# Kernel optimization log

Measured on AMD Instinct MI355X. Metric: run time of the kernel, lower is better.

Reference implementation:

```python
import jax, jax.numpy as jnp
import numpy as np

B, H, L, TAU, THETA = 8192, 256, 4, 8, 8


def setup_inputs() -> dict:
    key = jax.random.key(0)
    ks = jax.random.split(key, 16)
    w = lambda k, shape: (jax.random.normal(k, shape, jnp.float32) * 0.02)
    return {
        "x": jax.random.normal(ks[0], (B, H), jnp.float32),
        "t_att": jax.random.normal(ks[1], (L, TAU, B, H), jnp.float32),
        "s_att": jax.random.normal(ks[2], (L, TAU, B, H), jnp.float32),
        "embed_w": w(ks[3], (H, H)),
        "embed_b": jnp.zeros((H,), jnp.float32),
        "wtn": w(ks[4], (L, H, H)),
        "btn": jnp.zeros((L, H), jnp.float32),
        "wsn": w(ks[5], (L, H, H)),
        "bsn": jnp.zeros((L, H), jnp.float32),
        "wt": w(ks[6], (L, 3 * H, H)),
        "bt": jnp.zeros((L, 3 * H), jnp.float32),
        "ws": w(ks[7], (L, 3 * H, H)),
        "bs": jnp.zeros((L, 3 * H), jnp.float32),
        "out_w": w(ks[8], (H, H)),
        "out_b": jnp.zeros((H,), jnp.float32),
    }


def _forward(x, t_att, s_att, embed_w, embed_b, wtn, btn, wsn, bsn, wt, bt, ws, bs, out_w, out_b):
    n_layers, tau = t_att.shape[0], t_att.shape[1]
    b, h = x.shape
    scale = 1.0 / np.sqrt(h).astype(np.float32)
    theta = THETA

    S = x @ embed_w.T + embed_b  # embed: [B, H]
    # rolling spatial buffers, start as theta zero entries
    t_sp = jnp.zeros((theta, b, h), x.dtype)
    s_sp = jnp.zeros((theta, b, h), x.dtype)

    for i in range(n_layers):
        T_last = t_att[i, -1]  # [B, H]
        # append current S_t / last T_t to spatial buffers, keep last theta
        s_sp = jnp.concatenate([s_sp[1:], S[None]], axis=0)
        t_sp = jnp.concatenate([t_sp[1:], T_last[None]], axis=0)
        # s_att[i].append(S_t); slice last tau -> keys include current S
        s_keys = jnp.concatenate([s_att[i, 1:], S[None]], axis=0)  # [tau, B, H]
        t_vals = t_att[i]  # [tau, B, H]

        s_next = S @ wsn[i].T + bsn[i]
        t_next = T_last @ wtn[i].T + btn[i]

        # temporal attention over last-tau history
        w_t = jax.nn.softmax(jnp.einsum('kbh,bh->kb', s_keys, s_next) * scale, axis=0)
        T_trend = jnp.einsum('kb,kbh->bh', w_t, t_vals)
        t_gate = jax.nn.sigmoid(t_next)
        T_fusion = T_last * t_gate + (1.0 - t_gate) * T_trend

        # spatial attention over last-theta buffer
        w_s = jax.nn.softmax(jnp.einsum('kbh,bh->kb', t_sp, t_next) * scale, axis=0)
        S_trend = jnp.einsum('kb,kbh->bh', w_s, s_sp)
        s_gate = jax.nn.sigmoid(s_next)
        S_fusion = S * s_gate + (1.0 - s_gate) * S_trend

        Tc = T_fusion @ wt[i].T + bt[i]  # [B, 3H]
        Sc = S_fusion @ ws[i].T + bs[i]
        t_g, t_t_, t_s_ = jnp.split(Tc, 3, axis=-1)
        s_g, s_t_, s_s_ = jnp.split(Sc, 3, axis=-1)
        Tg = jax.nn.sigmoid(t_g)
        Sg = jax.nn.sigmoid(s_g)
        # T_new feeds the (stateful) history; S carries to next layer
        S = Sg * s_s_ + (1.0 - Sg) * t_s_

    return jnp.tanh(S @ out_w.T + out_b)


def reference(x, t_att, s_att, embed_w, embed_b, wtn, btn, wsn, bsn, wt, bt, ws, bs, out_w, out_b):
    return _forward(x, t_att, s_att, embed_w, embed_b, wtn, btn, wsn, bsn, wt, bt, ws, bs, out_w, out_b)
```

## Files before the change

kernel.cpp:

```cpp
#include <hip/hip_runtime.h>
#include <cmath>

typedef __attribute__((ext_vector_type(8))) short short8;
typedef __attribute__((ext_vector_type(4))) float f32x4;
typedef __attribute__((ext_vector_type(4))) unsigned short us4;
typedef unsigned short u16;

#define BATCH 8192
#define HDIM  256
static constexpr size_t BH = (size_t)BATCH * HDIM;

__device__ __forceinline__ u16 f2bf(float f) {
    union { float f; unsigned u; } v; v.f = f;
    unsigned r = v.u + 0x7FFFu + ((v.u >> 16) & 1u);
    return (u16)(r >> 16);
}
__device__ __forceinline__ float bf2f(u16 u) {
    union { unsigned u; float f; } v; v.u = ((unsigned)u) << 16;
    return v.f;
}
__device__ __forceinline__ float wred(float v) {
#pragma unroll
    for (int o = 32; o > 0; o >>= 1) v += __shfl_xor(v, o);
    return v;
}
__device__ __forceinline__ float sigmoidf_(float x) {
    return 1.f / (1.f + __expf(-x));
}

__global__ __launch_bounds__(256) void convert_weights(
    const float* __restrict__ embed_w, const float* __restrict__ wtn,
    const float* __restrict__ wsn, const float* __restrict__ wt,
    const float* __restrict__ ws, const float* __restrict__ out_w,
    u16* __restrict__ dst)
{
    int idx = blockIdx.x * 256 + threadIdx.x;
    int e = idx * 4;
    if (e >= 22 * 65536) return;
    int c = e >> 16, o = e & 65535;
    const float* src;
    if (c == 0)      src = embed_w + o;
    else if (c < 5)  src = wtn + (size_t)(c - 1) * 65536 + o;
    else if (c < 9)  src = wsn + (size_t)(c - 5) * 65536 + o;
    else if (c < 13) src = wt + (size_t)(c - 9) * 768 * 256 + 512 * 256 + o;
    else if (c < 17) src = ws + (size_t)(c - 13) * 768 * 256 + o;
    else if (c < 21) src = ws + (size_t)(c - 17) * 768 * 256 + 512 * 256 + o;
    else             src = out_w + o;
    f32x4 v = *(const f32x4*)src;
    us4 r;
#pragma unroll
    for (int j = 0; j < 4; ++j) r[j] = f2bf(v[j]);
    *(us4*)(dst + e) = r;
}

template<bool A_F32, int ACT>
__global__ __launch_bounds__(256) void gemm256(
    const void* __restrict__ Ap, const u16* __restrict__ W,
    const float* __restrict__ bias, void* __restrict__ Cp)
{
    int lane = threadIdx.x & 63;
    int wave = threadIdx.x >> 6;
    int wm = wave >> 1, wn = wave & 1;
    int row0 = blockIdx.x * 128 + wm * 64;
    int col0 = blockIdx.y * 64 + wn * 32;
    int lr = lane & 15;
    int kg = lane >> 4;

    f32x4 acc[4][2] = {};
    for (int k0 = 0; k0 < 256; k0 += 32) {
        int k = k0 + kg * 8;
        short8 a[4], b[2];
        if constexpr (A_F32) {
            const float* A = (const float*)Ap;
#pragma unroll
            for (int mt = 0; mt < 4; ++mt) {
                const float* p = A + (size_t)(row0 + mt * 16 + lr) * 256 + k;
                f32x4 lo = *(const f32x4*)p;
                f32x4 hi = *(const f32x4*)(p + 4);
                short8 t;
                t[0] = (short)f2bf(lo[0]); t[1] = (short)f2bf(lo[1]);
                t[2] = (short)f2bf(lo[2]); t[3] = (short)f2bf(lo[3]);
                t[4] = (short)f2bf(hi[0]); t[5] = (short)f2bf(hi[1]);
                t[6] = (short)f2bf(hi[2]); t[7] = (short)f2bf(hi[3]);
                a[mt] = t;
            }
        } else {
            const u16* A = (const u16*)Ap;
#pragma unroll
            for (int mt = 0; mt < 4; ++mt)
                a[mt] = *(const short8*)(A + (size_t)(row0 + mt * 16 + lr) * 256 + k);
        }
#pragma unroll
        for (int nt = 0; nt < 2; ++nt)
            b[nt] = *(const short8*)(W + (size_t)(col0 + nt * 16 + lr) * 256 + k);
#pragma unroll
        for (int mt = 0; mt < 4; ++mt)
#pragma unroll
            for (int nt = 0; nt < 2; ++nt)
                acc[mt][nt] = __builtin_amdgcn_mfma_f32_16x16x32_bf16(a[mt], b[nt], acc[mt][nt], 0, 0, 0);
    }
#pragma unroll
    for (int nt = 0; nt < 2; ++nt) {
        int n = col0 + nt * 16 + lr;
        float bn = bias[n];
#pragma unroll
        for (int mt = 0; mt < 4; ++mt) {
            int m0 = row0 + mt * 16 + kg * 4;
#pragma unroll
            for (int r = 0; r < 4; ++r) {
                float v = acc[mt][nt][r] + bn;
                if constexpr (ACT == 0) ((u16*)Cp)[(size_t)(m0 + r) * 256 + n] = f2bf(v);
                else                    ((float*)Cp)[(size_t)(m0 + r) * 256 + n] = tanhf(v);
            }
        }
    }
}

__global__ __launch_bounds__(256) void gemm_fuse3(
    const u16* __restrict__ Tf, const u16* __restrict__ Sf,
    const u16* __restrict__ Wt3, const u16* __restrict__ Ws1, const u16* __restrict__ Ws3,
    const float* __restrict__ bt3, const float* __restrict__ bs1, const float* __restrict__ bs3,
    u16* __restrict__ Sout)
{
    int lane = threadIdx.x & 63;
    int wave = threadIdx.x >> 6;
    int wm = wave >> 1, wn = wave & 1;
    int row0 = blockIdx.x * 128 + wm * 64;
    int col0 = blockIdx.y * 64 + wn * 32;
    int lr = lane & 15;
    int kg = lane >> 4;

    f32x4 accT[4][2] = {}, accG[4][2] = {}, accS[4][2] = {};
    for (int k0 = 0; k0 < 256; k0 += 32) {
        int k = k0 + kg * 8;
        short8 at[4], as[4], bT[2], bG[2], bS[2];
#pragma unroll
        for (int mt = 0; mt < 4; ++mt) {
            size_t off = (size_t)(row0 + mt * 16 + lr) * 256 + k;
            at[mt] = *(const short8*)(Tf + off);
            as[mt] = *(const short8*)(Sf + off);
        }
#pragma unroll
        for (int nt = 0; nt < 2; ++nt) {
            size_t off = (size_t)(col0 + nt * 16 + lr) * 256 + k;
            bT[nt] = *(const short8*)(Wt3 + off);
            bG[nt] = *(const short8*)(Ws1 + off);
            bS[nt] = *(const short8*)(Ws3 + off);
        }
#pragma unroll
        for (int mt = 0; mt < 4; ++mt)
#pragma unroll
            for (int nt = 0; nt < 2; ++nt) {
                accT[mt][nt] = __builtin_amdgcn_mfma_f32_16x16x32_bf16(at[mt], bT[nt], accT[mt][nt], 0, 0, 0);
                accG[mt][nt] = __builtin_amdgcn_mfma_f32_16x16x32_bf16(as[mt], bG[nt], accG[mt][nt], 0, 0, 0);
                accS[mt][nt] = __builtin_amdgcn_mfma_f32_16x16x32_bf16(as[mt], bS[nt], accS[mt][nt], 0, 0, 0);
            }
    }
#pragma unroll
    for (int nt = 0; nt < 2; ++nt) {
        int n = col0 + nt * 16 + lr;
        float b1 = bt3[n], b2 = bs1[n], b3 = bs3[n];
#pragma unroll
        for (int mt = 0; mt < 4; ++mt) {
            int m0 = row0 + mt * 16 + kg * 4;
#pragma unroll
            for (int r = 0; r < 4; ++r) {
                float g = sigmoidf_(accG[mt][nt][r] + b2);
                float v = g * (accS[mt][nt][r] + b3) + (1.f - g) * (accT[mt][nt][r] + b1);
                Sout[(size_t)(m0 + r) * 256 + n] = f2bf(v);
            }
        }
    }
}

__global__ __launch_bounds__(256) void attn_fuse(
    const float* __restrict__ t_att, const float* __restrict__ s_att,
    const u16* __restrict__ S_hist,
    const u16* __restrict__ s_next, const u16* __restrict__ t_next,
    u16* __restrict__ T_fus, u16* __restrict__ S_fus, int layer)
{
    const int b = blockIdx.x * 4 + (threadIdx.x >> 6);
    const int lane = threadIdx.x & 63;
    const size_t rowoff = (size_t)b * 256 + lane * 4;
    const float scale = 0.0625f;

    us4 snu = *(const us4*)(s_next + rowoff);
    us4 tnu = *(const us4*)(t_next + rowoff);
    us4 scu = *(const us4*)(S_hist + (size_t)layer * BH + rowoff);
    float sn[4], tn[4], Sc[4];
#pragma unroll
    for (int j = 0; j < 4; ++j) { sn[j] = bf2f(snu[j]); tn[j] = bf2f(tnu[j]); Sc[j] = bf2f(scu[j]); }

    const float* ta = t_att + (size_t)layer * 8 * BH + rowoff;
    const float* sa = s_att + (size_t)layer * 8 * BH + rowoff;

    float lt[8];
#pragma unroll
    for (int kk = 0; kk < 7; ++kk) {
        f32x4 v = *(const f32x4*)(sa + (size_t)(kk + 1) * BH);
        lt[kk] = wred(v[0] * sn[0] + v[1] * sn[1] + v[2] * sn[2] + v[3] * sn[3]) * scale;
    }
    lt[7] = wred(Sc[0] * sn[0] + Sc[1] * sn[1] + Sc[2] * sn[2] + Sc[3] * sn[3]) * scale;

    float m = lt[0];
#pragma unroll
    for (int kk = 1; kk < 8; ++kk) m = fmaxf(m, lt[kk]);
    float w8[8], den = 0.f;
#pragma unroll
    for (int kk = 0; kk < 8; ++kk) { w8[kk] = __expf(lt[kk] - m); den += w8[kk]; }
    float inv = 1.f / den;

    float Tt[4] = {0.f, 0.f, 0.f, 0.f}, Tl[4];
#pragma unroll
    for (int kk = 0; kk < 8; ++kk) {
        f32x4 v = *(const f32x4*)(ta + (size_t)kk * BH);
#pragma unroll
        for (int j = 0; j < 4; ++j) Tt[j] += w8[kk] * v[j];
        if (kk == 7) { Tl[0] = v[0]; Tl[1] = v[1]; Tl[2] = v[2]; Tl[3] = v[3]; }
    }
    us4 ot;
#pragma unroll
    for (int j = 0; j < 4; ++j) {
        float g = sigmoidf_(tn[j]);
        ot[j] = f2bf(Tl[j] * g + (1.f - g) * Tt[j] * inv);
    }
    *(us4*)(T_fus + rowoff) = ot;

    float msx = 0.f;
    float dens = (float)(7 - layer);
    float St[4] = {0.f, 0.f, 0.f, 0.f};
    for (int jj = 0; jj <= layer; ++jj) {
        f32x4 v = *(const f32x4*)(t_att + ((size_t)jj * 8 + 7) * BH + rowoff);
        float p = wred(v[0] * tn[0] + v[1] * tn[1] + v[2] * tn[2] + v[3] * tn[3]) * scale;
        us4 shu = *(const us4*)(S_hist + (size_t)jj * BH + rowoff);
        if (p > msx) {
            float c = __expf(msx - p);
            dens *= c; St[0] *= c; St[1] *= c; St[2] *= c; St[3] *= c;
            msx = p;
        }
        float w = __expf(p - msx);
        dens += w;
#pragma unroll
        for (int j = 0; j < 4; ++j) St[j] += w * bf2f(shu[j]);
    }
    float invs = 1.f / dens;
    us4 os;
#pragma unroll
    for (int j = 0; j < 4; ++j) {
        float g = sigmoidf_(sn[j]);
        os[j] = f2bf(Sc[j] * g + (1.f - g) * St[j] * invs);
    }
    *(us4*)(S_fus + rowoff) = os;
}

extern "C" void kernel_launch(void* const* d_in, const int* in_sizes, int n_in,
                              void* d_out, int out_size, void* d_ws, size_t ws_size,
                              hipStream_t stream)
{
    (void)in_sizes; (void)n_in; (void)out_size; (void)ws_size;
    const float* x       = (const float*)d_in[0];
    const float* t_att   = (const float*)d_in[1];
    const float* s_att   = (const float*)d_in[2];
    const float* embed_w = (const float*)d_in[3];
    const float* embed_b = (const float*)d_in[4];
    const float* wtn     = (const float*)d_in[5];
    const float* btn     = (const float*)d_in[6];
    const float* wsn     = (const float*)d_in[7];
    const float* bsn     = (const float*)d_in[8];
    const float* wt      = (const float*)d_in[9];
    const float* bt      = (const float*)d_in[10];
    const float* ws_in   = (const float*)d_in[11];
    const float* bs      = (const float*)d_in[12];
    const float* out_w   = (const float*)d_in[13];
    const float* out_b   = (const float*)d_in[14];

    u16* wsp     = (u16*)d_ws;
    u16* Wbf     = wsp;
    u16* S_hist  = wsp + (size_t)22 * 65536;
    u16* s_next  = S_hist + 5 * BH;
    u16* t_next  = s_next + BH;
    u16* T_fus   = t_next + BH;
    u16* S_fus   = T_fus + BH;

    u16* embed_w_bf = Wbf;
    u16* wtn_bf     = Wbf + (size_t)1  * 65536;
    u16* wsn_bf     = Wbf + (size_t)5  * 65536;
    u16* wt3_bf     = Wbf + (size_t)9  * 65536;
    u16* ws1_bf     = Wbf + (size_t)13 * 65536;
    u16* ws3_bf     = Wbf + (size_t)17 * 65536;
    u16* out_w_bf   = Wbf + (size_t)21 * 65536;

    convert_weights<<<1408, 256, 0, stream>>>(embed_w, wtn, wsn, wt, ws_in, out_w, Wbf);

    dim3 gg(BATCH / 128, HDIM / 64);

    gemm256<true, 0><<<gg, 256, 0, stream>>>(x, embed_w_bf, embed_b, S_hist);

    for (int i = 0; i < 4; ++i) {
        gemm256<false, 0><<<gg, 256, 0, stream>>>(S_hist + (size_t)i * BH,
                                                  wsn_bf + (size_t)i * 65536,
                                                  bsn + i * 256, s_next);
        gemm256<true, 0><<<gg, 256, 0, stream>>>(t_att + ((size_t)i * 8 + 7) * BH,
                                                 wtn_bf + (size_t)i * 65536,
                                                 btn + i * 256, t_next);
        attn_fuse<<<BATCH / 4, 256, 0, stream>>>(t_att, s_att, S_hist, s_next, t_next,
                                                 T_fus, S_fus, i);
        gemm_fuse3<<<gg, 256, 0, stream>>>(T_fus, S_fus,
                                           wt3_bf + (size_t)i * 65536,
                                           ws1_bf + (size_t)i * 65536,
                                           ws3_bf + (size_t)i * 65536,
                                           bt + i * 768 + 512, bs + i * 768, bs + i * 768 + 512,
                                           S_hist + (size_t)(i + 1) * BH);
    }

    gemm256<false, 1><<<gg, 256, 0, stream>>>(S_hist + (size_t)4 * BH, out_w_bf, out_b, d_out);
}
```

Measured before the change: 308.2 us.

## Fuse per-layer projections, attention and gated GEMM into one kernel

Merges the two next-state GEMMs, the attention/fusion step and the three-way gated GEMM of each layer into a single kernel that handles 16 batch rows per block. The intermediate s_next/t_next, T_fus and S_fus stay in shared memory instead of going through global memory, which removes four launches per layer and their round-trips. The embed and output GEMMs are retiled so each block covers the full N dimension. The trade-off is that each block now reads every weight matrix in full for only 16 rows, so weight traffic from cache rises and occupancy may drop because of the shared memory use.

```diff
diff --git a/kernel.cpp b/kernel.cpp
--- a/kernel.cpp
+++ b/kernel.cpp
@@ -54,22 +54,21 @@
 }
 
 template<bool A_F32, int ACT>
-__global__ __launch_bounds__(256) void gemm256(
+__global__ __launch_bounds__(256) void gemm_fullN(
     const void* __restrict__ Ap, const u16* __restrict__ W,
     const float* __restrict__ bias, void* __restrict__ Cp)
 {
-    int lane = threadIdx.x & 63;
-    int wave = threadIdx.x >> 6;
-    int wm = wave >> 1, wn = wave & 1;
-    int row0 = blockIdx.x * 128 + wm * 64;
-    int col0 = blockIdx.y * 64 + wn * 32;
-    int lr = lane & 15;
-    int kg = lane >> 4;
-
-    f32x4 acc[4][2] = {};
+    const int lane = threadIdx.x & 63;
+    const int wave = threadIdx.x >> 6;
+    const int row0 = blockIdx.x * 64;
+    const int n0 = wave * 64;
+    const int lr = lane & 15;
+    const int kg = lane >> 4;
+
+    f32x4 acc[4][4] = {};
     for (int k0 = 0; k0 < 256; k0 += 32) {
         int k = k0 + kg * 8;
-        short8 a[4], b[2];
+        short8 a[4], b[4];
         if constexpr (A_F32) {
             const float* A = (const float*)Ap;
 #pragma unroll
@@ -91,17 +90,17 @@
                 a[mt] = *(const short8*)(A + (size_t)(row0 + mt * 16 + lr) * 256 + k);
         }
 #pragma unroll
-        for (int nt = 0; nt < 2; ++nt)
-            b[nt] = *(const short8*)(W + (size_t)(col0 + nt * 16 + lr) * 256 + k);
+        for (int nt = 0; nt < 4; ++nt)
+            b[nt] = *(const short8*)(W + (size_t)(n0 + nt * 16 + lr) * 256 + k);
 #pragma unroll
         for (int mt = 0; mt < 4; ++mt)
 #pragma unroll
-            for (int nt = 0; nt < 2; ++nt)
+            for (int nt = 0; nt < 4; ++nt)
                 acc[mt][nt] = __builtin_amdgcn_mfma_f32_16x16x32_bf16(a[mt], b[nt], acc[mt][nt], 0, 0, 0);
     }
 #pragma unroll
-    for (int nt = 0; nt < 2; ++nt) {
-        int n = col0 + nt * 16 + lr;
+    for (int nt = 0; nt < 4; ++nt) {
+        int n = n0 + nt * 16 + lr;
         float bn = bias[n];
 #pragma unroll
         for (int mt = 0; mt < 4; ++mt) {
@@ -116,141 +115,181 @@
     }
 }
 
-__global__ __launch_bounds__(256) void gemm_fuse3(
-    const u16* __restrict__ Tf, const u16* __restrict__ Sf,
-    const u16* __restrict__ Wt3, const u16* __restrict__ Ws1, const u16* __restrict__ Ws3,
-    const float* __restrict__ bt3, const float* __restrict__ bs1, const float* __restrict__ bs3,
-    u16* __restrict__ Sout)
+#define SNP 260
+#define TFP 264
+__global__ __launch_bounds__(256) void layer_fused(
+    const float* __restrict__ t_att, const float* __restrict__ s_att,
+    u16* __restrict__ S_hist, const u16* __restrict__ Wbf,
+    const float* __restrict__ btn, const float* __restrict__ bsn,
+    const float* __restrict__ bt, const float* __restrict__ bs,
+    int layer)
 {
-    int lane = threadIdx.x & 63;
-    int wave = threadIdx.x >> 6;
-    int wm = wave >> 1, wn = wave & 1;
-    int row0 = blockIdx.x * 128 + wm * 64;
-    int col0 = blockIdx.y * 64 + wn * 32;
-    int lr = lane & 15;
-    int kg = lane >> 4;
-
-    f32x4 accT[4][2] = {}, accG[4][2] = {}, accS[4][2] = {};
-    for (int k0 = 0; k0 < 256; k0 += 32) {
-        int k = k0 + kg * 8;
-        short8 at[4], as[4], bT[2], bG[2], bS[2];
-#pragma unroll
-        for (int mt = 0; mt < 4; ++mt) {
-            size_t off = (size_t)(row0 + mt * 16 + lr) * 256 + k;
-            at[mt] = *(const short8*)(Tf + off);
-            as[mt] = *(const short8*)(Sf + off);
-        }
-#pragma unroll
-        for (int nt = 0; nt < 2; ++nt) {
-            size_t off = (size_t)(col0 + nt * 16 + lr) * 256 + k;
-            bT[nt] = *(const short8*)(Wt3 + off);
-            bG[nt] = *(const short8*)(Ws1 + off);
-            bS[nt] = *(const short8*)(Ws3 + off);
-        }
-#pragma unroll
-        for (int mt = 0; mt < 4; ++mt)
-#pragma unroll
-            for (int nt = 0; nt < 2; ++nt) {
-                accT[mt][nt] = __builtin_amdgcn_mfma_f32_16x16x32_bf16(at[mt], bT[nt], accT[mt][nt], 0, 0, 0);
-                accG[mt][nt] = __builtin_amdgcn_mfma_f32_16x16x32_bf16(as[mt], bG[nt], accG[mt][nt], 0, 0, 0);
-                accS[mt][nt] = __builtin_amdgcn_mfma_f32_16x16x32_bf16(as[mt], bS[nt], accS[mt][nt], 0, 0, 0);
-            }
-    }
-#pragma unroll
-    for (int nt = 0; nt < 2; ++nt) {
-        int n = col0 + nt * 16 + lr;
-        float b1 = bt3[n], b2 = bs1[n], b3 = bs3[n];
-#pragma unroll
-        for (int mt = 0; mt < 4; ++mt) {
-            int m0 = row0 + mt * 16 + kg * 4;
+    __shared__ float sn_lds[16 * SNP];
+    __shared__ float tn_lds[16 * SNP];
+    __shared__ u16   tf_lds[16 * TFP];
+    __shared__ u16   sf_lds[16 * TFP];
+
+    const int lane = threadIdx.x & 63;
+    const int wave = threadIdx.x >> 6;
+    const int lr = lane & 15;
+    const int kg = lane >> 4;
+    const int row0 = blockIdx.x * 16;
+
+    {
+        const int g = wave >> 1;
+        const int n0 = (wave & 1) * 128;
+        const u16* Wm = Wbf + (size_t)((g ? 1 : 5) + layer) * 65536;
+        const float* bias = (g ? btn : bsn) + layer * 256;
+        const u16* Abf = S_hist + (size_t)layer * BH;
+        const float* Af = t_att + ((size_t)layer * 8 + 7) * BH;
+
+        f32x4 acc[8] = {};
+        for (int k0 = 0; k0 < 256; k0 += 32) {
+            int k = k0 + kg * 8;
+            short8 a;
+            if (g == 0) {
+                a = *(const short8*)(Abf + (size_t)(row0 + lr) * 256 + k);
+            } else {
+                const float* p = Af + (size_t)(row0 + lr) * 256 + k;
+                f32x4 lo = *(const f32x4*)p;
+                f32x4 hi = *(const f32x4*)(p + 4);
+                short8 t;
+                t[0] = (short)f2bf(lo[0]); t[1] = (short)f2bf(lo[1]);
+                t[2] = (short)f2bf(lo[2]); t[3] = (short)f2bf(lo[3]);
+                t[4] = (short)f2bf(hi[0]); t[5] = (short)f2bf(hi[1]);
+                t[6] = (short)f2bf(hi[2]); t[7] = (short)f2bf(hi[3]);
+                a = t;
+            }
+#pragma unroll
+            for (int nf = 0; nf < 8; ++nf) {
+                short8 b = *(const short8*)(Wm + (size_t)(n0 + nf * 16 + lr) * 256 + k);
+                acc[nf] = __builtin_amdgcn_mfma_f32_16x16x32_bf16(a, b, acc[nf], 0, 0, 0);
+            }
+        }
+        float* dst = g ? tn_lds : sn_lds;
+#pragma unroll
+        for (int nf = 0; nf < 8; ++nf) {
+            int n = n0 + nf * 16 + lr;
+            float bn = bias[n];
+#pragma unroll
+            for (int r = 0; r < 4; ++r)
+                dst[(kg * 4 + r) * SNP + n] = acc[nf][r] + bn;
+        }
+    }
+    __syncthreads();
+
+    {
+        const float scale = 0.0625f;
+        for (int rr = wave * 4; rr < wave * 4 + 4; ++rr) {
+            const int b = row0 + rr;
+            const size_t ro = (size_t)b * 256 + lane * 4;
+
+            f32x4 snv = *(const f32x4*)(sn_lds + rr * SNP + lane * 4);
+            f32x4 tnv = *(const f32x4*)(tn_lds + rr * SNP + lane * 4);
+            us4 scu = *(const us4*)(S_hist + (size_t)layer * BH + ro);
+            float Sc[4];
+#pragma unroll
+            for (int j = 0; j < 4; ++j) Sc[j] = bf2f(scu[j]);
+
+            const float* ta = t_att + (size_t)layer * 8 * BH + ro;
+            const float* sa = s_att + (size_t)layer * 8 * BH + ro;
+
+            float lt[8];
+#pragma unroll
+            for (int kk = 0; kk < 7; ++kk) {
+                f32x4 v = *(const f32x4*)(sa + (size_t)(kk + 1) * BH);
+                lt[kk] = wred(v[0] * snv[0] + v[1] * snv[1] + v[2] * snv[2] + v[3] * snv[3]) * scale;
+            }
+            lt[7] = wred(Sc[0] * snv[0] + Sc[1] * snv[1] + Sc[2] * snv[2] + Sc[3] * snv[3]) * scale;
+
+            float m = lt[0];
+#pragma unroll
+            for (int kk = 1; kk < 8; ++kk) m = fmaxf(m, lt[kk]);
+            float w8[8], den = 0.f;
+#pragma unroll
+            for (int kk = 0; kk < 8; ++kk) { w8[kk] = __expf(lt[kk] - m); den += w8[kk]; }
+            float inv = 1.f / den;
+
+            float Tt[4] = {0.f, 0.f, 0.f, 0.f}, Tl[4];
+#pragma unroll
+            for (int kk = 0; kk < 8; ++kk) {
+                f32x4 v = *(const f32x4*)(ta + (size_t)kk * BH);
+#pragma unroll
+                for (int j = 0; j < 4; ++j) Tt[j] += w8[kk] * v[j];
+                if (kk == 7) { Tl[0] = v[0]; Tl[1] = v[1]; Tl[2] = v[2]; Tl[3] = v[3]; }
+            }
+            us4 ot;
+#pragma unroll
+            for (int j = 0; j < 4; ++j) {
+                float g = sigmoidf_(tnv[j]);
+                ot[j] = f2bf(Tl[j] * g + (1.f - g) * Tt[j] * inv);
+            }
+            *(us4*)(tf_lds + rr * TFP + lane * 4) = ot;
+
+            float msx = 0.f;
+            float dens = (float)(7 - layer);
+            float St[4] = {0.f, 0.f, 0.f, 0.f};
+            for (int jj = 0; jj <= layer; ++jj) {
+                f32x4 v = *(const f32x4*)(t_att + ((size_t)jj * 8 + 7) * BH + ro);
+                float p = wred(v[0] * tnv[0] + v[1] * tnv[1] + v[2] * tnv[2] + v[3] * tnv[3]) * scale;
+                us4 shu = *(const us4*)(S_hist + (size_t)jj * BH + ro);
+                if (p > msx) {
+                    float c = __expf(msx - p);
+                    dens *= c; St[0] *= c; St[1] *= c; St[2] *= c; St[3] *= c;
+                    msx = p;
+                }
+                float w = __expf(p - msx);
+                dens += w;
+#pragma unroll
+                for (int j = 0; j < 4; ++j) St[j] += w * bf2f(shu[j]);
+            }
+            float invs = 1.f / dens;
+            us4 os;
+#pragma unroll
+            for (int j = 0; j < 4; ++j) {
+                float g = sigmoidf_(snv[j]);
+                os[j] = f2bf(Sc[j] * g + (1.f - g) * St[j] * invs);
+            }
+            *(us4*)(sf_lds + rr * TFP + lane * 4) = os;
+        }
+    }
+    __syncthreads();
+
+    {
+        const int n0 = wave * 64;
+        const u16* Wt3 = Wbf + (size_t)(9  + layer) * 65536;
+        const u16* Ws1 = Wbf + (size_t)(13 + layer) * 65536;
+        const u16* Ws3 = Wbf + (size_t)(17 + layer) * 65536;
+
+        f32x4 accT[4] = {}, accG[4] = {}, accS[4] = {};
+        for (int k0 = 0; k0 < 256; k0 += 32) {
+            int k = k0 + kg * 8;
+            short8 at = *(const short8*)(tf_lds + lr * TFP + k);
+            short8 as = *(const short8*)(sf_lds + lr * TFP + k);
+#pragma unroll
+            for (int nf = 0; nf < 4; ++nf) {
+                size_t wo = (size_t)(n0 + nf * 16 + lr) * 256 + k;
+                accT[nf] = __builtin_amdgcn_mfma_f32_16x16x32_bf16(at, *(const short8*)(Wt3 + wo), accT[nf], 0, 0, 0);
+                accG[nf] = __builtin_amdgcn_mfma_f32_16x16x32_bf16(as, *(const short8*)(Ws1 + wo), accG[nf], 0, 0, 0);
+                accS[nf] = __builtin_amdgcn_mfma_f32_16x16x32_bf16(as, *(const short8*)(Ws3 + wo), accS[nf], 0, 0, 0);
+            }
+        }
+        u16* Sout = S_hist + (size_t)(layer + 1) * BH;
+        const float* b1 = bt + layer * 768 + 512;
+        const float* b2 = bs + layer * 768;
+        const float* b3 = bs + layer * 768 + 512;
+#pragma unroll
+        for (int nf = 0; nf < 4; ++nf) {
+            int n = n0 + nf * 16 + lr;
+            float bb1 = b1[n], bb2 = b2[n], bb3 = b3[n];
 #pragma unroll
             for (int r = 0; r < 4; ++r) {
-                float g = sigmoidf_(accG[mt][nt][r] + b2);
-                float v = g * (accS[mt][nt][r] + b3) + (1.f - g) * (accT[mt][nt][r] + b1);
-                Sout[(size_t)(m0 + r) * 256 + n] = f2bf(v);
-            }
-        }
-    }
-}
-
-__global__ __launch_bounds__(256) void attn_fuse(
-    const float* __restrict__ t_att, const float* __restrict__ s_att,
-    const u16* __restrict__ S_hist,
-    const u16* __restrict__ s_next, const u16* __restrict__ t_next,
-    u16* __restrict__ T_fus, u16* __restrict__ S_fus, int layer)
-{
-    const int b = blockIdx.x * 4 + (threadIdx.x >> 6);
-    const int lane = threadIdx.x & 63;
-    const size_t rowoff = (size_t)b * 256 + lane * 4;
-    const float scale = 0.0625f;
-
-    us4 snu = *(const us4*)(s_next + rowoff);
-    us4 tnu = *(const us4*)(t_next + rowoff);
-    us4 scu = *(const us4*)(S_hist + (size_t)layer * BH + rowoff);
-    float sn[4], tn[4], Sc[4];
-#pragma unroll
-    for (int j = 0; j < 4; ++j) { sn[j] = bf2f(snu[j]); tn[j] = bf2f(tnu[j]); Sc[j] = bf2f(scu[j]); }
-
-    const float* ta = t_att + (size_t)layer * 8 * BH + rowoff;
-    const float* sa = s_att + (size_t)layer * 8 * BH + rowoff;
-
-    float lt[8];
-#pragma unroll
-    for (int kk = 0; kk < 7; ++kk) {
-        f32x4 v = *(const f32x4*)(sa + (size_t)(kk + 1) * BH);
-        lt[kk] = wred(v[0] * sn[0] + v[1] * sn[1] + v[2] * sn[2] + v[3] * sn[3]) * scale;
-    }
-    lt[7] = wred(Sc[0] * sn[0] + Sc[1] * sn[1] + Sc[2] * sn[2] + Sc[3] * sn[3]) * scale;
-
-    float m = lt[0];
-#pragma unroll
-    for (int kk = 1; kk < 8; ++kk) m = fmaxf(m, lt[kk]);
-    float w8[8], den = 0.f;
-#pragma unroll
-    for (int kk = 0; kk < 8; ++kk) { w8[kk] = __expf(lt[kk] - m); den += w8[kk]; }
-    float inv = 1.f / den;
-
-    float Tt[4] = {0.f, 0.f, 0.f, 0.f}, Tl[4];
-#pragma unroll
-    for (int kk = 0; kk < 8; ++kk) {
-        f32x4 v = *(const f32x4*)(ta + (size_t)kk * BH);
-#pragma unroll
-        for (int j = 0; j < 4; ++j) Tt[j] += w8[kk] * v[j];
-        if (kk == 7) { Tl[0] = v[0]; Tl[1] = v[1]; Tl[2] = v[2]; Tl[3] = v[3]; }
-    }
-    us4 ot;
-#pragma unroll
-    for (int j = 0; j < 4; ++j) {
-        float g = sigmoidf_(tn[j]);
-        ot[j] = f2bf(Tl[j] * g + (1.f - g) * Tt[j] * inv);
-    }
-    *(us4*)(T_fus + rowoff) = ot;
-
-    float msx = 0.f;
-    float dens = (float)(7 - layer);
-    float St[4] = {0.f, 0.f, 0.f, 0.f};
-    for (int jj = 0; jj <= layer; ++jj) {
-        f32x4 v = *(const f32x4*)(t_att + ((size_t)jj * 8 + 7) * BH + rowoff);
-        float p = wred(v[0] * tn[0] + v[1] * tn[1] + v[2] * tn[2] + v[3] * tn[3]) * scale;
-        us4 shu = *(const us4*)(S_hist + (size_t)jj * BH + rowoff);
-        if (p > msx) {
-            float c = __expf(msx - p);
-            dens *= c; St[0] *= c; St[1] *= c; St[2] *= c; St[3] *= c;
-            msx = p;
-        }
-        float w = __expf(p - msx);
-        dens += w;
-#pragma unroll
-        for (int j = 0; j < 4; ++j) St[j] += w * bf2f(shu[j]);
-    }
-    float invs = 1.f / dens;
-    us4 os;
-#pragma unroll
-    for (int j = 0; j < 4; ++j) {
-        float g = sigmoidf_(sn[j]);
-        os[j] = f2bf(Sc[j] * g + (1.f - g) * St[j] * invs);
-    }
-    *(us4*)(S_fus + rowoff) = os;
+                float gv = sigmoidf_(accG[nf][r] + bb2);
+                float v = gv * (accS[nf][r] + bb3) + (1.f - gv) * (accT[nf][r] + bb1);
+                Sout[(size_t)(row0 + kg * 4 + r) * 256 + n] = f2bf(v);
+            }
+        }
+    }
 }
 
 extern "C" void kernel_launch(void* const* d_in, const int* in_sizes, int n_in,
@@ -274,44 +313,18 @@
     const float* out_w   = (const float*)d_in[13];
     const float* out_b   = (const float*)d_in[14];
 
-    u16* wsp     = (u16*)d_ws;
-    u16* Wbf     = wsp;
-    u16* S_hist  = wsp + (size_t)22 * 65536;
-    u16* s_next  = S_hist + 5 * BH;
-    u16* t_next  = s_next + BH;
-    u16* T_fus   = t_next + BH;
-    u16* S_fus   = T_fus + BH;
-
-    u16* embed_w_bf = Wbf;
-    u16* wtn_bf     = Wbf + (size_t)1  * 65536;
-    u16* wsn_bf     = Wbf + (size_t)5  * 65536;
-    u16* wt3_bf     = Wbf + (size_t)9  * 65536;
-    u16* ws1_bf     = Wbf + (size_t)13 * 65536;
-    u16* ws3_bf     = Wbf + (size_t)17 * 65536;
-    u16* out_w_bf   = Wbf + (size_t)21 * 65536;
+    u16* wsp    = (u16*)d_ws;
+    u16* Wbf    = wsp;
+    u16* S_hist = wsp + (size_t)22 * 65536;
 
     convert_weights<<<1408, 256, 0, stream>>>(embed_w, wtn, wsn, wt, ws_in, out_w, Wbf);
 
-    dim3 gg(BATCH / 128, HDIM / 64);
-
-    gemm256<true, 0><<<gg, 256, 0, stream>>>(x, embed_w_bf, embed_b, S_hist);
-
-    for (int i = 0; i < 4; ++i) {
-        gemm256<false, 0><<<gg, 256, 0, stream>>>(S_hist + (size_t)i * BH,
-                                                  wsn_bf + (size_t)i * 65536,
-                                                  bsn + i * 256, s_next);
-        gemm256<true, 0><<<gg, 256, 0, stream>>>(t_att + ((size_t)i * 8 + 7) * BH,
-                                                 wtn_bf + (size_t)i * 65536,
-                                                 btn + i * 256, t_next);
-        attn_fuse<<<BATCH / 4, 256, 0, stream>>>(t_att, s_att, S_hist, s_next, t_next,
-                                                 T_fus, S_fus, i);
-        gemm_fuse3<<<gg, 256, 0, stream>>>(T_fus, S_fus,
-                                           wt3_bf + (size_t)i * 65536,
-                                           ws1_bf + (size_t)i * 65536,
-                                           ws3_bf + (size_t)i * 65536,
-                                           bt + i * 768 + 512, bs + i * 768, bs + i * 768 + 512,
-                                           S_hist + (size_t)(i + 1) * BH);
-    }
-
-    gemm256<false, 1><<<gg, 256, 0, stream>>>(S_hist + (size_t)4 * BH, out_w_bf, out_b, d_out);
-}
+    gemm_fullN<true, 0><<<BATCH / 64, 256, 0, stream>>>(x, Wbf, embed_b, S_hist);
+
+    for (int i = 0; i < 4; ++i)
+        layer_fused<<<BATCH / 16, 256, 0, stream>>>(t_att, s_att, S_hist, Wbf,
+                                                    btn, bsn, bt, bs, i);
+
+    gemm_fullN<false, 1><<<BATCH / 64, 256, 0, stream>>>(
+        S_hist + (size_t)4 * BH, Wbf + (size_t)21 * 65536, out_b, d_out);
+}
```

Result: slower. 335.3 us (+8.8%).
